# Optimization experiments

Measured on AMD Instinct MI355X. Metric: run time of the kernel, lower is better.

The kernel has to match this reference:

```python
import jax, jax.numpy as jnp
import numpy as np

K, D, BETA = 512, 64, 0.25


def conv(x, w, b, s, p):
    # x: NCHW, w: OIHW (torch Conv2d layout)
    y = jax.lax.conv_general_dilated(x, w, (s, s), [(p, p), (p, p)],
                                     dimension_numbers=('NCHW', 'OIHW', 'NCHW'))
    if b is not None:
        y = y + b[None, :, None, None]
    return y


def conv_t(x, w, b, s, p):
    # torch ConvTranspose2d: w is (Cin, Cout, k, k). Equivalent to a dilated conv
    # with flipped, transposed kernel and padding k-1-p.
    k = w.shape[2]
    w2 = jnp.transpose(jnp.flip(w, (2, 3)), (1, 0, 2, 3))  # -> (Cout, Cin, k, k)
    y = jax.lax.conv_general_dilated(x, w2, (1, 1), [(k - 1 - p, k - 1 - p)] * 2,
                                     lhs_dilation=(s, s),
                                     dimension_numbers=('NCHW', 'OIHW', 'NCHW'))
    return y + b[None, :, None, None]


def res_stack(x, w1s, w2s):
    # w1s: (n_blocks, C_mid, C_in, 3, 3); w2s: (n_blocks, C_in, C_mid, 1, 1); no bias
    for i in range(w1s.shape[0]):
        h = conv(jax.nn.relu(x), w1s[i], None, 1, 1)
        h = conv(jax.nn.relu(h), w2s[i], None, 1, 0)
        x = x + h
    return jax.nn.relu(x)


def setup_inputs() -> dict:
    key = jax.random.key(0)
    ks = jax.random.split(key, 24)
    rn = lambda k, shape, s=0.05: (jax.random.normal(k, shape, jnp.float32) * s)
    return {
        'x': jax.random.normal(ks[0], (64, 3, 128, 128), jnp.float32),
        'enc_w1': rn(ks[1], (64, 3, 4, 4)),    'enc_b1': rn(ks[2], (64,)),
        'enc_w2': rn(ks[3], (128, 64, 4, 4)),  'enc_b2': rn(ks[4], (128,)),
        'enc_w3': rn(ks[5], (128, 128, 3, 3)), 'enc_b3': rn(ks[6], (128,)),
        'enc_w4': rn(ks[7], (128, 128, 3, 3)), 'enc_b4': rn(ks[8], (128,)),
        'enc_res_w1': rn(ks[9], (2, 64, 128, 3, 3)),
        'enc_res_w2': rn(ks[10], (2, 128, 64, 1, 1)),
        'enc_adj_w': rn(ks[11], (64, 128, 1, 1)), 'enc_adj_b': rn(ks[12], (64,)),
        'E': jax.random.uniform(ks[13], (K, D), jnp.float32, -1.0 / K, 1.0 / K),
        'dec_adj_w': rn(ks[14], (128, 64, 3, 3)), 'dec_adj_b': rn(ks[15], (128,)),
        'dec_res_w1': rn(ks[16], (2, 64, 128, 3, 3)),
        'dec_res_w2': rn(ks[17], (2, 128, 64, 1, 1)),
        'tc1_w': rn(ks[18], (128, 64, 4, 4)), 'tc1_b': rn(ks[19], (64,)),
        'tc2_w': rn(ks[20], (64, 3, 4, 4)),  'tc2_b': rn(ks[21], (3,)),
    }


def vq_vae_forward(x, enc_w1, enc_b1, enc_w2, enc_b2, enc_w3, enc_b3, enc_w4, enc_b4,
                   enc_res_w1, enc_res_w2, enc_adj_w, enc_adj_b, E,
                   dec_adj_w, dec_adj_b, dec_res_w1, dec_res_w2, tc1_w, tc1_b, tc2_w, tc2_b):
    relu = jax.nn.relu
    # ---- Encoder ----
    h = relu(conv(x, enc_w1, enc_b1, 2, 1))      # (B,64,64,64)
    h = relu(conv(h, enc_w2, enc_b2, 2, 1))      # (B,128,32,32)
    h = relu(conv(h, enc_w3, enc_b3, 1, 1))
    h = conv(h, enc_w4, enc_b4, 1, 1)
    h = res_stack(h, enc_res_w1, enc_res_w2)
    Ze = conv(h, enc_adj_w, enc_adj_b, 1, 0)     # (B,D,32,32)
    # ---- Vector quantizer (eval mode, use_EMA=False) ----
    Zt = jnp.transpose(Ze, (0, 2, 3, 1))          # (B,H,W,D)
    flat = Zt.reshape(-1, D)                      # (N,D), N=65536
    dist = (jnp.sum(flat ** 2, axis=1, keepdims=True)
            + jnp.sum(E ** 2, axis=1)
            - 2.0 * flat @ E.T)                    # (N,K)
    idx = jnp.argmin(dist, axis=1)                # (N,)
    Zq = E[idx].reshape(Zt.shape)
    e_latent_loss = jnp.mean((jax.lax.stop_gradient(Zq) - Zt) ** 2)
    q_latent_loss = jnp.mean((Zq - jax.lax.stop_gradient(Zt)) ** 2)
    e_and_q = q_latent_loss + BETA * e_latent_loss
    Zq_st = Zt + jax.lax.stop_gradient(Zq - Zt)   # straight-through
    Zq_nchw = jnp.transpose(Zq_st, (0, 3, 1, 2))
    counts = jnp.zeros((K,), jnp.float32).at[idx].add(1.0)
    probs = counts / jnp.sum(counts)
    entropy_bits = -jnp.sum(probs * jnp.log2(probs + 1e-10))  # zero-count terms vanish
    est_words = 2.0 ** entropy_bits
    # ---- Decoder ----
    g = conv(Zq_nchw, dec_adj_w, dec_adj_b, 1, 1)  # (B,128,32,32)
    g = res_stack(g, dec_res_w1, dec_res_w2)
    g = relu(conv_t(g, tc1_w, tc1_b, 2, 1))        # (B,64,64,64)
    x_recon = conv_t(g, tc2_w, tc2_b, 2, 1)        # (B,3,128,128)
    return e_and_q, x_recon, e_latent_loss, q_latent_loss, est_words


def reference(x, enc_w1, enc_b1, enc_w2, enc_b2, enc_w3, enc_b3, enc_w4, enc_b4,
              enc_res_w1, enc_res_w2, enc_adj_w, enc_adj_b, E,
              dec_adj_w, dec_adj_b, dec_res_w1, dec_res_w2, tc1_w, tc1_b, tc2_w, tc2_b):
    return vq_vae_forward(x, enc_w1, enc_b1, enc_w2, enc_b2, enc_w3, enc_b3, enc_w4, enc_b4,
                          enc_res_w1, enc_res_w2, enc_adj_w, enc_adj_b, E,
                          dec_adj_w, dec_adj_b, dec_res_w1, dec_res_w2, tc1_w, tc1_b, tc2_w, tc2_b)
```

## Files before the change

kernel.cpp:

```cpp
#include <hip/hip_runtime.h>
#include <math.h>


typedef unsigned short u16;
typedef __attribute__((ext_vector_type(8))) short bf16x8;
typedef __attribute__((ext_vector_type(4))) float f32x4;

__device__ __forceinline__ float bf2f(u16 h) {
    union { unsigned u; float f; } v; v.u = ((unsigned)h) << 16; return v.f;
}
__device__ __forceinline__ u16 f2bf(float f) {
    union { float f; unsigned u; } v; v.f = f;
    unsigned r = v.u + 0x7FFFu + ((v.u >> 16) & 1u);
    return (u16)(r >> 16);
}
__device__ __forceinline__ unsigned relu2(unsigned x) {
    return x & ~(((x & 0x80008000u) >> 15) * 0xFFFFu);
}

template<int CIN, int COUT, int TAPMODE, bool RELU_IN, bool RELU_OUT,
         bool HAS_BIAS, bool RESID>
__global__ __launch_bounds__(256)
void mfma_conv_k(const u16* __restrict__ in, const u16* __restrict__ wT,
                 const float* __restrict__ bias, u16* __restrict__ out,
                 int Hin, int Win, int Hout, int Wout, int OS)
{
    constexpr int TM = 2, TN = 4;
    constexpr int LDA = 40;
    constexpr int NCH = CIN / 32;
    constexpr int NTAPS = (TAPMODE == 0) ? 1 : (TAPMODE == 1) ? 9
                        : (TAPMODE == 2) ? 16 : 4;
    constexpr int S = (TAPMODE == 2) ? 2 : 1;

    __shared__ alignas(16) u16 aT[128 * LDA];
    __shared__ alignas(16) u16 bT[64 * LDA];

    const int tid = threadIdx.x;
    const int m0 = blockIdx.x * 128;
    const int colbase = blockIdx.y << 6;
    const int pz = (TAPMODE == 3) ? blockIdx.z : 0;
    const u16* wTb = (TAPMODE == 3) ? wT + (size_t)pz * 4 * COUT * CIN : wT;
    const int oph = (TAPMODE == 3) ? (pz >> 1) : 0;
    const int opw = (TAPMODE == 3) ? (pz & 1) : 0;
    const int n_img = m0 >> 10;
    const int pixbase = m0 & 1023;

    const int r = tid >> 1, half = tid & 1;
    const int pr = pixbase + r;
    const int ohr = pr >> 5, owr = pr & 31;
    const u16* inb = in + (size_t)n_img * Hin * Win * CIN;

    const int wv = tid >> 6, lane = tid & 63;
    const int q = lane >> 4, l16 = lane & 15;
    const int mbase = wv * 32;
    const bool bload = r < 64;

    f32x4 acc[TM][TN] = {};

    const int total_it = NTAPS * NCH;
    uint4 pa0, pa1, pb0 = {0,0,0,0}, pb1 = {0,0,0,0};

#define LOAD_IT(IT) do {                                                        \
        int t_ = (IT) / NCH, cc_ = ((IT) % NCH) * 32;                           \
        int dh_, dw_;                                                           \
        if (TAPMODE == 0)      { dh_ = 0;              dw_ = 0; }               \
        else if (TAPMODE == 1) { dh_ = t_/3 - 1;       dw_ = t_%3 - 1; }        \
        else if (TAPMODE == 2) { dh_ = (t_>>2) - 1;    dw_ = (t_&3) - 1; }      \
        else                   { dh_ = (pz>>1) - (t_>>1); dw_ = (pz&1) - (t_&1); } \
        int ih_ = ohr * S + dh_;                                                \
        int iw_ = owr * S + dw_;                                                \
        bool ok_ = ((unsigned)ih_ < (unsigned)Hin) &&                           \
                   ((unsigned)iw_ < (unsigned)Win);                             \
        pa0 = (uint4){0,0,0,0}; pa1 = (uint4){0,0,0,0};                         \
        if (ok_) {                                                              \
            const u16* as_ = inb + ((size_t)ih_ * Win + iw_) * CIN              \
                             + half * 16 + cc_;                                 \
            pa0 = *(const uint4*)(as_);                                         \
            pa1 = *(const uint4*)(as_ + 8);                                     \
        }                                                                       \
        if (bload) {                                                            \
            const u16* bs_ = wTb + ((size_t)t_ * COUT + colbase + r) * CIN      \
                             + half * 16 + cc_;                                 \
            pb0 = *(const uint4*)(bs_);                                         \
            pb1 = *(const uint4*)(bs_ + 8);                                     \
        }                                                                       \
    } while (0)

    LOAD_IT(0);

    for (int it = 0; it < total_it; ++it) {
        __syncthreads();
        uint4 a0 = pa0, a1 = pa1;
        if (RELU_IN) {
            a0.x = relu2(a0.x); a0.y = relu2(a0.y); a0.z = relu2(a0.z); a0.w = relu2(a0.w);
            a1.x = relu2(a1.x); a1.y = relu2(a1.y); a1.z = relu2(a1.z); a1.w = relu2(a1.w);
        }
        *(uint4*)&aT[r * LDA + half * 16]     = a0;
        *(uint4*)&aT[r * LDA + half * 16 + 8] = a1;
        if (bload) {
            *(uint4*)&bT[r * LDA + half * 16]     = pb0;
            *(uint4*)&bT[r * LDA + half * 16 + 8] = pb1;
        }
        __syncthreads();
        if (it + 1 < total_it) LOAD_IT(it + 1);

        bf16x8 afr[TM], bfr[TN];
        #pragma unroll
        for (int tm = 0; tm < TM; ++tm)
            afr[tm] = *(const bf16x8*)&aT[(mbase + tm*16 + l16) * LDA + q * 8];
        #pragma unroll
        for (int tn = 0; tn < TN; ++tn)
            bfr[tn] = *(const bf16x8*)&bT[(tn*16 + l16) * LDA + q * 8];
        #pragma unroll
        for (int tm = 0; tm < TM; ++tm)
            #pragma unroll
            for (int tn = 0; tn < TN; ++tn)
                acc[tm][tn] = __builtin_amdgcn_mfma_f32_16x16x32_bf16(
                    afr[tm], bfr[tn], acc[tm][tn], 0, 0, 0);
    }
#undef LOAD_IT

    #pragma unroll
    for (int tm = 0; tm < TM; ++tm) {
        #pragma unroll
        for (int tn = 0; tn < TN; ++tn) {
            const int col = colbase + tn*16 + l16;
            const float bv = HAS_BIAS ? bias[col] : 0.0f;
            #pragma unroll
            for (int rg = 0; rg < 4; ++rg) {
                const int m = mbase + tm*16 + q*4 + rg;
                const int pix = pixbase + m;
                const int oh = pix >> 5, ow = pix & 31;
                size_t oidx = (((size_t)n_img * Hout + (oh*OS + oph)) * Wout
                               + (ow*OS + opw)) * COUT + col;
                float v = acc[tm][tn][rg] + bv;
                if (RESID) v += bf2f(out[oidx]);
                if (RELU_OUT) v = fmaxf(v, 0.0f);
                out[oidx] = f2bf(v);
            }
        }
    }
}

__global__ __launch_bounds__(256)
void res_fused_k(const u16* __restrict__ in, const u16* __restrict__ w1,
                 const u16* __restrict__ w2, u16* __restrict__ out)
{
    constexpr int LDA = 40;
    __shared__ alignas(16) u16 smem[20480];
    u16* aT   = smem;
    u16* bT   = smem + 5120;
    u16* mT0  = smem;
    u16* mT1  = smem + 5120;
    u16* b2T0 = smem + 10240;
    u16* b2T1 = smem + 15360;

    const int tid = threadIdx.x;
    const int m0 = blockIdx.x * 128;
    const int n_img = m0 >> 10;
    const int pixbase = m0 & 1023;

    const int r = tid >> 1, half = tid & 1;
    const int pr = pixbase + r;
    const int ohr = pr >> 5, owr = pr & 31;
    const u16* inb = in + (size_t)n_img * 1024 * 128;

    const int wv = tid >> 6, lane = tid & 63;
    const int q = lane >> 4, l16 = lane & 15;
    const int mbase = wv * 32;
    const bool bload = r < 64;

    {
        const u16* s = w2 + r * 64 + half * 32;
        u16* d = (half ? b2T1 : b2T0) + r * LDA;
        *(uint4*)(d)      = *(const uint4*)(s);
        *(uint4*)(d + 8)  = *(const uint4*)(s + 8);
        *(uint4*)(d + 16) = *(const uint4*)(s + 16);
        *(uint4*)(d + 24) = *(const uint4*)(s + 24);
    }

    f32x4 acc[2][4] = {};
    uint4 pa0, pa1, pb0 = {0,0,0,0}, pb1 = {0,0,0,0};

#define RLOAD(IT) do {                                                          \
        int t_ = (IT) >> 2, cc_ = ((IT) & 3) * 32;                              \
        int ih_ = ohr + t_/3 - 1, iw_ = owr + t_%3 - 1;                         \
        bool ok_ = ((unsigned)ih_ < 32u) && ((unsigned)iw_ < 32u);              \
        pa0 = (uint4){0,0,0,0}; pa1 = (uint4){0,0,0,0};                         \
        if (ok_) {                                                              \
            const u16* as_ = inb + ((size_t)ih_ * 32 + iw_) * 128               \
                             + half * 16 + cc_;                                 \
            pa0 = *(const uint4*)(as_);                                         \
            pa1 = *(const uint4*)(as_ + 8);                                     \
        }                                                                       \
        if (bload) {                                                            \
            const u16* bs_ = w1 + ((size_t)t_ * 64 + r) * 128                   \
                             + half * 16 + cc_;                                 \
            pb0 = *(const uint4*)(bs_);                                         \
            pb1 = *(const uint4*)(bs_ + 8);                                     \
        }                                                                       \
    } while (0)

    RLOAD(0);
    for (int it = 0; it < 36; ++it) {
        __syncthreads();
        uint4 a0 = pa0, a1 = pa1;
        a0.x = relu2(a0.x); a0.y = relu2(a0.y); a0.z = relu2(a0.z); a0.w = relu2(a0.w);
        a1.x = relu2(a1.x); a1.y = relu2(a1.y); a1.z = relu2(a1.z); a1.w = relu2(a1.w);
        *(uint4*)&aT[r * LDA + half * 16]     = a0;
        *(uint4*)&aT[r * LDA + half * 16 + 8] = a1;
        if (bload) {
            *(uint4*)&bT[r * LDA + half * 16]     = pb0;
            *(uint4*)&bT[r * LDA + half * 16 + 8] = pb1;
        }
        __syncthreads();
        if (it + 1 < 36) RLOAD(it + 1);

        bf16x8 afr[2], bfr[4];
        #pragma unroll
        for (int tm = 0; tm < 2; ++tm)
            afr[tm] = *(const bf16x8*)&aT[(mbase + tm*16 + l16) * LDA + q * 8];
        #pragma unroll
        for (int tn = 0; tn < 4; ++tn)
            bfr[tn] = *(const bf16x8*)&bT[(tn*16 + l16) * LDA + q * 8];
        #pragma unroll
        for (int tm = 0; tm < 2; ++tm)
            #pragma unroll
            for (int tn = 0; tn < 4; ++tn)
                acc[tm][tn] = __builtin_amdgcn_mfma_f32_16x16x32_bf16(
                    afr[tm], bfr[tn], acc[tm][tn], 0, 0, 0);
    }
#undef RLOAD

    __syncthreads();

    #pragma unroll
    for (int tm = 0; tm < 2; ++tm)
        #pragma unroll
        for (int tn = 0; tn < 4; ++tn) {
            u16* dst = (tn < 2) ? mT0 : mT1;
            const int kc = (tn & 1) * 16 + l16;
            #pragma unroll
            for (int rg = 0; rg < 4; ++rg) {
                int row = mbase + tm*16 + q*4 + rg;
                dst[row * LDA + kc] = f2bf(fmaxf(acc[tm][tn][rg], 0.0f));
            }
        }
    __syncthreads();

    f32x4 acc2[2][8] = {};
    #pragma unroll
    for (int kk = 0; kk < 2; ++kk) {
        const u16* mp = kk ? mT1 : mT0;
        const u16* bp = kk ? b2T1 : b2T0;
        bf16x8 af[2], bf[8];
        #pragma unroll
        for (int tm = 0; tm < 2; ++tm)
            af[tm] = *(const bf16x8*)&mp[(mbase + tm*16 + l16) * LDA + q * 8];
        #pragma unroll
        for (int tn = 0; tn < 8; ++tn)
            bf[tn] = *(const bf16x8*)&bp[(tn*16 + l16) * LDA + q * 8];
        #pragma unroll
        for (int tm = 0; tm < 2; ++tm)
            #pragma unroll
            for (int tn = 0; tn < 8; ++tn)
                acc2[tm][tn] = __builtin_amdgcn_mfma_f32_16x16x32_bf16(
                    af[tm], bf[tn], acc2[tm][tn], 0, 0, 0);
    }

    #pragma unroll
    for (int tm = 0; tm < 2; ++tm)
        #pragma unroll
        for (int tn = 0; tn < 8; ++tn) {
            const int col = tn*16 + l16;
            #pragma unroll
            for (int rg = 0; rg < 4; ++rg) {
                const int m = mbase + tm*16 + q*4 + rg;
                const int pix = pixbase + m;
                size_t off = ((size_t)n_img * 1024 + pix) * 128 + col;
                out[off] = f2bf(acc2[tm][tn][rg] + bf2f(in[off]));
            }
        }
}

__global__ __launch_bounds__(256)
void adjvq_k(const u16* __restrict__ TRin, const u16* __restrict__ wadj,
             const float* __restrict__ bias, const u16* __restrict__ Ebf,
             const float* __restrict__ enorm1, u16* __restrict__ Zq,
             u16* __restrict__ idx_out, float* __restrict__ sse)
{
    constexpr int LDA = 40;
    __shared__ alignas(16) u16 smem[18432];
    u16* aT  = smem;
    u16* bT  = smem + 5120;
    u16* mT0 = smem;
    u16* mT1 = smem + 5120;
    u16* eld = smem;
    __shared__ float znorm_s[128];
    __shared__ float bestf_s[128];
    __shared__ float en1s[256];
    __shared__ int   bestk_s[128];
    __shared__ float red[256];

    const int tid = threadIdx.x;
    const int r = tid >> 1, half = tid & 1;
    const size_t gp = (size_t)blockIdx.x * 128 + r;
    const u16* arow = TRin + gp * 128 + half * 16;
    const u16* brow = wadj + (size_t)r * 128 + half * 16;

    const int wv = tid >> 6, lane = tid & 63;
    const int q = lane >> 4, l16 = lane & 15;
    const int mbase = wv * 32;

    f32x4 acc[2][4] = {};
    for (int c0 = 0; c0 < 128; c0 += 32) {
        __syncthreads();
        uint4 a0 = *(const uint4*)(arow + c0);
        uint4 a1 = *(const uint4*)(arow + c0 + 8);
        a0.x = relu2(a0.x); a0.y = relu2(a0.y); a0.z = relu2(a0.z); a0.w = relu2(a0.w);
        a1.x = relu2(a1.x); a1.y = relu2(a1.y); a1.z = relu2(a1.z); a1.w = relu2(a1.w);
        *(uint4*)&aT[r * LDA + half * 16]     = a0;
        *(uint4*)&aT[r * LDA + half * 16 + 8] = a1;
        if (r < 64) {
            *(uint4*)&bT[r * LDA + half * 16]     = *(const uint4*)(brow + c0);
            *(uint4*)&bT[r * LDA + half * 16 + 8] = *(const uint4*)(brow + c0 + 8);
        }
        __syncthreads();
        bf16x8 afr[2], bfr[4];
        #pragma unroll
        for (int tm = 0; tm < 2; ++tm)
            afr[tm] = *(const bf16x8*)&aT[(mbase + tm*16 + l16) * LDA + q * 8];
        #pragma unroll
        for (int tn = 0; tn < 4; ++tn)
            bfr[tn] = *(const bf16x8*)&bT[(tn*16 + l16) * LDA + q * 8];
        #pragma unroll
        for (int tm = 0; tm < 2; ++tm)
            #pragma unroll
            for (int tn = 0; tn < 4; ++tn)
                acc[tm][tn] = __builtin_amdgcn_mfma_f32_16x16x32_bf16(
                    afr[tm], bfr[tn], acc[tm][tn], 0, 0, 0);
    }

    float zn[2][4] = {};
    #pragma unroll
    for (int tm = 0; tm < 2; ++tm)
        #pragma unroll
        for (int tn = 0; tn < 4; ++tn) {
            const float bv = bias[tn*16 + l16];
            #pragma unroll
            for (int rg = 0; rg < 4; ++rg) {
                float z = acc[tm][tn][rg] + bv;
                acc[tm][tn][rg] = z;
                zn[tm][rg] = fmaf(z, z, zn[tm][rg]);
            }
        }
    #pragma unroll
    for (int m = 1; m < 16; m <<= 1)
        #pragma unroll
        for (int tm = 0; tm < 2; ++tm)
            #pragma unroll
            for (int rg = 0; rg < 4; ++rg)
                zn[tm][rg] += __shfl_xor(zn[tm][rg], m, 64);

    __syncthreads();

    #pragma unroll
    for (int tm = 0; tm < 2; ++tm) {
        #pragma unroll
        for (int tn = 0; tn < 4; ++tn) {
            u16* dst = (tn < 2) ? mT0 : mT1;
            const int kc = (tn & 1) * 16 + l16;
            #pragma unroll
            for (int rg = 0; rg < 4; ++rg) {
                int row = mbase + tm*16 + q*4 + rg;
                dst[row * LDA + kc] = f2bf(acc[tm][tn][rg]);
            }
        }
        if (l16 == 0)
            #pragma unroll
            for (int rg = 0; rg < 4; ++rg)
                znorm_s[mbase + tm*16 + q*4 + rg] = zn[tm][rg];
    }
    __syncthreads();

    bf16x8 alo[2], ahi[2];
    #pragma unroll
    for (int tile = 0; tile < 2; ++tile) {
        alo[tile] = *(const bf16x8*)&mT0[(mbase + tile*16 + l16) * LDA + q * 8];
        ahi[tile] = *(const bf16x8*)&mT1[(mbase + tile*16 + l16) * LDA + q * 8];
    }

    unsigned key[2][4] = {{0xFFFFFFFFu,0xFFFFFFFFu,0xFFFFFFFFu,0xFFFFFFFFu},
                          {0xFFFFFFFFu,0xFFFFFFFFu,0xFFFFFFFFu,0xFFFFFFFFu}};
    float fb[2][4] = {{1e30f,1e30f,1e30f,1e30f},{1e30f,1e30f,1e30f,1e30f}};

    for (int k0 = 0; k0 < 512; k0 += 256) {
        __syncthreads();
        const uint4* src = (const uint4*)(Ebf + k0 * 64);
        #pragma unroll
        for (int i = tid; i < 2048; i += 256) {
            int row = i >> 3, sub = i & 7;
            *(uint4*)&eld[row * 72 + sub * 8] = src[i];
        }
        en1s[tid] = enorm1[k0 + tid];
        __syncthreads();

        for (int t = 0; t < 16; ++t) {
            const int nl = t * 16 + l16;
            bf16x8 b0 = *(const bf16x8*)&eld[nl * 72 + q * 8];
            bf16x8 b1 = *(const bf16x8*)&eld[nl * 72 + 32 + q * 8];
            const float en1 = en1s[nl];
            const unsigned ng = (unsigned)(k0 + nl);
            #pragma unroll
            for (int tile = 0; tile < 2; ++tile) {
                f32x4 sc4 = {0.0f, 0.0f, 0.0f, 0.0f};
                sc4 = __builtin_amdgcn_mfma_f32_16x16x32_bf16(alo[tile], b0, sc4, 0, 0, 0);
                sc4 = __builtin_amdgcn_mfma_f32_16x16x32_bf16(ahi[tile], b1, sc4, 0, 0, 0);
                #pragma unroll
                for (int rg = 0; rg < 4; ++rg) {
                    float sc = fmaf(sc4[rg], -2.0f, en1);
                    unsigned kk2 = (__float_as_uint(sc) & 0xFFFFFE00u) | ng;
                    key[tile][rg] = min(key[tile][rg], kk2);
                    fb[tile][rg] = fminf(fb[tile][rg], sc);
                }
            }
        }
    }

    #pragma unroll
    for (int m = 1; m < 16; m <<= 1)
        #pragma unroll
        for (int tile = 0; tile < 2; ++tile)
            #pragma unroll
            for (int rg = 0; rg < 4; ++rg) {
                unsigned o = (unsigned)__shfl_xor((int)key[tile][rg], m, 64);
                key[tile][rg] = min(key[tile][rg], o);
                float of = __shfl_xor(fb[tile][rg], m, 64);
                fb[tile][rg] = fminf(fb[tile][rg], of);
            }
    if (l16 == 0)
        #pragma unroll
        for (int tile = 0; tile < 2; ++tile)
            #pragma unroll
            for (int rg = 0; rg < 4; ++rg) {
                int row = mbase + tile*16 + q*4 + rg;
                bestk_s[row] = (int)(key[tile][rg] & 511u);
                bestf_s[row] = fb[tile][rg];
            }
    __syncthreads();

    const int pos = tid >> 1, seg = tid & 1;
    const size_t p = (size_t)blockIdx.x * 128 + pos;
    const int k = bestk_s[pos];
    const u16* ep = Ebf + (size_t)k * 64 + seg * 32;
    u16* qp = Zq + p * 64 + seg * 32;
    #pragma unroll
    for (int h = 0; h < 4; ++h)
        *(uint4*)(qp + h * 8) = *(const uint4*)(ep + h * 8);
    if (seg == 0) idx_out[p] = (u16)k;
    red[tid] = (seg == 0) ? (znorm_s[pos] + bestf_s[pos] - 1.0f) : 0.0f;
    __syncthreads();
    for (int s = 128; s > 0; s >>= 1) {
        if (tid < s) red[tid] += red[tid + s];
        __syncthreads();
    }
    if (tid == 0) atomicAdd(sse, red[0]);
}

__global__ __launch_bounds__(256)
void conv1_mfma_k(const float* __restrict__ x, const u16* __restrict__ wc1b,
                  const float* __restrict__ b, u16* __restrict__ out)
{
    __shared__ alignas(16) u16 smem[15360];
    u16* aT0 = smem;
    u16* aT1 = smem + 5120;
    u16* bT0 = smem + 10240;
    u16* bT1 = smem + 12800;

    const int tid = threadIdx.x;
    const int gbase = blockIdx.x * 128;
    const int r = tid >> 1, half = tid & 1;
    const int p = gbase + r;
    const int ow = p & 63, oh = (p >> 6) & 63, n = p >> 12;
    const float* xb = x + (size_t)n * 3 * 16384;

    {
        int row = tid >> 2, sub = tid & 3;
        *(uint4*)&bT0[row*40 + sub*8] = *(const uint4*)(wc1b + row*64 + sub*8);
        *(uint4*)&bT1[row*40 + sub*8] = *(const uint4*)(wc1b + row*64 + 32 + sub*8);
    }

    float vals[24];
    const int kb = half * 24;
    #pragma unroll
    for (int j = 0; j < 24; ++j) {
        int k = kb + j;
        int ci = k >> 4, kh = (k >> 2) & 3, kw = k & 3;
        int ih = oh*2 - 1 + kh, iw = ow*2 - 1 + kw;
        bool ok = ((unsigned)ih < 128u) && ((unsigned)iw < 128u);
        vals[j] = ok ? xb[ci*16384 + ih*128 + iw] : 0.0f;
    }
    unsigned pk[12];
    #pragma unroll
    for (int jj = 0; jj < 12; ++jj)
        pk[jj] = (unsigned)f2bf(vals[2*jj]) | ((unsigned)f2bf(vals[2*jj+1]) << 16);
    unsigned* a0row = (unsigned*)&aT0[r * 40];
    unsigned* a1row = (unsigned*)&aT1[r * 40];
    if (half == 0) {
        #pragma unroll
        for (int jj = 0; jj < 12; ++jj) a0row[jj] = pk[jj];
    } else {
        a0row[12] = pk[0]; a0row[13] = pk[1];
        a0row[14] = pk[2]; a0row[15] = pk[3];
        #pragma unroll
        for (int jj = 4; jj < 12; ++jj) a1row[jj - 4] = pk[jj];
        *(uint4*)&aT1[r*40 + 16] = (uint4){0,0,0,0};
        *(uint4*)&aT1[r*40 + 24] = (uint4){0,0,0,0};
    }
    __syncthreads();

    const int wv = tid >> 6, lane = tid & 63;
    const int q = lane >> 4, l16 = lane & 15;
    const int mbase = wv * 32;

    f32x4 acc[2][4] = {};
    bf16x8 af0[2], af1[2], bf0[4], bf1[4];
    #pragma unroll
    for (int tm = 0; tm < 2; ++tm) {
        af0[tm] = *(const bf16x8*)&aT0[(mbase + tm*16 + l16) * 40 + q * 8];
        af1[tm] = *(const bf16x8*)&aT1[(mbase + tm*16 + l16) * 40 + q * 8];
    }
    #pragma unroll
    for (int tn = 0; tn < 4; ++tn) {
        bf0[tn] = *(const bf16x8*)&bT0[(tn*16 + l16) * 40 + q * 8];
        bf1[tn] = *(const bf16x8*)&bT1[(tn*16 + l16) * 40 + q * 8];
    }
    #pragma unroll
    for (int tm = 0; tm < 2; ++tm)
        #pragma unroll
        for (int tn = 0; tn < 4; ++tn) {
            acc[tm][tn] = __builtin_amdgcn_mfma_f32_16x16x32_bf16(
                af0[tm], bf0[tn], acc[tm][tn], 0, 0, 0);
            acc[tm][tn] = __builtin_amdgcn_mfma_f32_16x16x32_bf16(
                af1[tm], bf1[tn], acc[tm][tn], 0, 0, 0);
        }

    float bv[4];
    #pragma unroll
    for (int tn = 0; tn < 4; ++tn) bv[tn] = b[tn*16 + l16];

    __syncthreads();
    u16* cbuf = smem;
    #pragma unroll
    for (int tm = 0; tm < 2; ++tm)
        #pragma unroll
        for (int tn = 0; tn < 4; ++tn)
            #pragma unroll
            for (int rg = 0; rg < 4; ++rg) {
                int row = mbase + tm*16 + q*4 + rg;
                int col = tn*16 + l16;
                cbuf[row*72 + col] = f2bf(fmaxf(acc[tm][tn][rg] + bv[tn], 0.0f));
            }
    __syncthreads();

    u16* ob = out + (size_t)gbase * 64;
    #pragma unroll
    for (int it = 0; it < 4; ++it) {
        int j = it * 256 + tid;
        uint4 v = *(const uint4*)&cbuf[(j >> 3) * 72 + (j & 7) * 8];
        *(uint4*)(ob + j * 8) = v;
    }
}

__global__ __launch_bounds__(256)
void tc2_mfma_k(const u16* __restrict__ in, const u16* __restrict__ wT,
                const float* __restrict__ bias, float* __restrict__ out)
{
    constexpr int LDA = 40;
    __shared__ alignas(16) u16 aT[128 * LDA];
    __shared__ alignas(16) u16 bT[16 * LDA];
    __shared__ float cT[128 * 17];

    const int tid = threadIdx.x;
    const int m0 = blockIdx.x * 128;
    const int n_img = m0 >> 12;
    const int pixbase = m0 & 4095;
    const int y0 = pixbase >> 6;

    const int r = tid >> 1, half = tid & 1;
    const int pr = pixbase + r;
    const int yr = pr >> 6, xr = pr & 63;
    const u16* inb = in + (size_t)n_img * 4096 * 64;

    const int wv = tid >> 6, lane = tid & 63;
    const int q = lane >> 4, l16 = lane & 15;
    const int mbase = wv * 32;

    f32x4 acc[2] = {};

    for (int t = 0; t < 9; ++t) {
        const int ih = yr + t/3 - 1;
        const int iw = xr + t%3 - 1;
        const bool ok = ((unsigned)ih < 64u) && ((unsigned)iw < 64u);
        const u16* asrc = ok ? (inb + ((size_t)ih * 64 + iw) * 64 + half * 16) : inb;
        const u16* bsrc = wT + ((size_t)t * 16 + r) * 64 + half * 16;

        for (int c0 = 0; c0 < 64; c0 += 32) {
            __syncthreads();
            uint4 a0 = {0,0,0,0}, a1 = {0,0,0,0};
            if (ok) {
                a0 = *(const uint4*)(asrc + c0);
                a1 = *(const uint4*)(asrc + c0 + 8);
            }
            *(uint4*)&aT[r * LDA + half * 16]     = a0;
            *(uint4*)&aT[r * LDA + half * 16 + 8] = a1;
            if (r < 16) {
                *(uint4*)&bT[r * LDA + half * 16]     = *(const uint4*)(bsrc + c0);
                *(uint4*)&bT[r * LDA + half * 16 + 8] = *(const uint4*)(bsrc + c0 + 8);
            }
            __syncthreads();

            bf16x8 af0 = *(const bf16x8*)&aT[(mbase + l16) * LDA + q * 8];
            bf16x8 af1 = *(const bf16x8*)&aT[(mbase + 16 + l16) * LDA + q * 8];
            bf16x8 bf  = *(const bf16x8*)&bT[l16 * LDA + q * 8];
            acc[0] = __builtin_amdgcn_mfma_f32_16x16x32_bf16(af0, bf, acc[0], 0, 0, 0);
            acc[1] = __builtin_amdgcn_mfma_f32_16x16x32_bf16(af1, bf, acc[1], 0, 0, 0);
        }
    }

    #pragma unroll
    for (int tm = 0; tm < 2; ++tm)
        #pragma unroll
        for (int rg = 0; rg < 4; ++rg)
            cT[(mbase + tm*16 + q*4 + rg) * 17 + l16] = acc[tm][rg];
    __syncthreads();

    #pragma unroll
    for (int it = 0; it < 6; ++it) {
        int j = it * 256 + tid;
        int co  = j >> 9;
        int rem = j & 511;
        int ohl = rem >> 7;
        int ow  = rem & 127;
        int oh  = 2*y0 + ohl;
        int lp  = (ohl >> 1) * 64 + (ow >> 1);
        int col = ((ohl & 1) * 2 + (ow & 1)) * 4 + co;
        float v = cT[lp * 17 + col] + bias[co];
        out[(((size_t)n_img * 3 + co) * 128 + oh) * 128 + ow] = v;
    }
}

__global__ __launch_bounds__(256)
void hist_k(const u16* __restrict__ idx, float* __restrict__ counts)
{
    __shared__ int red[256];
    const int k = blockIdx.x;
    const int tid = threadIdx.x;
    int c = 0;
    const uint4* p4 = (const uint4*)idx;
    for (int i = tid; i < 8192; i += 256) {
        uint4 v = p4[i];
        unsigned ua[4] = {v.x, v.y, v.z, v.w};
        #pragma unroll
        for (int j = 0; j < 4; ++j) {
            c += ((ua[j] & 0xFFFFu) == (unsigned)k);
            c += ((ua[j] >> 16)     == (unsigned)k);
        }
    }
    red[tid] = c;
    __syncthreads();
    for (int s = 128; s > 0; s >>= 1) {
        if (tid < s) red[tid] += red[tid + s];
        __syncthreads();
    }
    if (tid == 0) counts[k] = (float)red[0];
}

__device__ __forceinline__ void wconv_tf(const float* __restrict__ w,
                                         u16* __restrict__ o,
                                         int COUT, int CIN, int KK, int i)
{
    int ci = i % CIN; int t = i / CIN; int co = t % COUT; t /= COUT;
    o[i] = f2bf(w[(co*CIN + ci)*KK + t]);
}

__global__ __launch_bounds__(256)
void prep_k(const float* __restrict__ enc_w1, const float* __restrict__ enc_w2,
            const float* __restrict__ enc_w3, const float* __restrict__ enc_w4,
            const float* __restrict__ enc_res_w1, const float* __restrict__ enc_res_w2,
            const float* __restrict__ dec_res_w1, const float* __restrict__ dec_res_w2,
            const float* __restrict__ enc_adj_w, const float* __restrict__ dec_adj_w,
            const float* __restrict__ tc1_w, const float* __restrict__ tc2_w,
            const float* __restrict__ E,
            u16* __restrict__ wc1b, u16* __restrict__ wc2, u16* __restrict__ wc3,
            u16* __restrict__ wc4, u16* __restrict__ wer1, u16* __restrict__ wer2,
            u16* __restrict__ wdr1, u16* __restrict__ wdr2, u16* __restrict__ weadj,
            u16* __restrict__ wdadj, u16* __restrict__ wtc1, u16* __restrict__ wtc2b,
            u16* __restrict__ Ebf, float* __restrict__ enorm1, float* __restrict__ sse)
{
    const int b = blockIdx.x, tid = threadIdx.x;
    if (b < 512) {
        wconv_tf(enc_w2, wc2, 128, 64, 16, b * 256 + tid);
    } else if (b < 1088) {
        wconv_tf(enc_w3, wc3, 128, 128, 9, (b - 512) * 256 + tid);
    } else if (b < 1664) {
        wconv_tf(enc_w4, wc4, 128, 128, 9, (b - 1088) * 256 + tid);
    } else if (b < 2240) {
        int i = (b - 1664) * 256 + tid;
        int sub = i / 73728, rem = i - sub * 73728;
        wconv_tf(enc_res_w1 + sub * 73728, wer1 + sub * 73728, 64, 128, 9, rem);
    } else if (b < 2816) {
        int i = (b - 2240) * 256 + tid;
        int sub = i / 73728, rem = i - sub * 73728;
        wconv_tf(dec_res_w1 + sub * 73728, wdr1 + sub * 73728, 64, 128, 9, rem);
    } else if (b < 2880) {
        int i = (b - 2816) * 256 + tid;
        int sub = i >> 13, rem = i & 8191;
        wconv_tf(enc_res_w2 + sub * 8192, wer2 + sub * 8192, 128, 64, 1, rem);
    } else if (b < 2944) {
        int i = (b - 2880) * 256 + tid;
        int sub = i >> 13, rem = i & 8191;
        wconv_tf(dec_res_w2 + sub * 8192, wdr2 + sub * 8192, 128, 64, 1, rem);
    } else if (b < 2976) {
        wconv_tf(enc_adj_w, weadj, 64, 128, 1, (b - 2944) * 256 + tid);
    } else if (b < 3264) {
        wconv_tf(dec_adj_w, wdadj, 128, 64, 9, (b - 2976) * 256 + tid);
    } else if (b < 3776) {
        int i = (b - 3264) * 256 + tid;
        int ci = i & 127; int co = (i >> 7) & 63; int t = (i >> 13) & 3; int p = i >> 15;
        int poh = p >> 1, pw = p & 1; int a = t >> 1, bb = t & 1;
        int kh = poh ? (a ? 2 : 0) : (a ? 3 : 1);
        int kw = pw  ? (bb ? 2 : 0) : (bb ? 3 : 1);
        wtc1[i] = f2bf(tc1_w[((ci*64 + co)*4 + kh)*4 + kw]);
    } else if (b < 3812) {
        int i = (b - 3776) * 256 + tid;
        int ci = i & 63; int col = (i >> 6) & 15; int t = i >> 10;
        int dh = t / 3 - 1, dw = t % 3 - 1;
        int pp = col >> 2, co = col & 3;
        float v = 0.0f;
        if (co < 3) {
            int poh = pp >> 1, pw = pp & 1;
            int kh = poh ? (dh == 1 ? 0 : (dh == 0 ? 2 : -1))
                         : (dh == 0 ? 1 : (dh == -1 ? 3 : -1));
            int kw = pw  ? (dw == 1 ? 0 : (dw == 0 ? 2 : -1))
                         : (dw == 0 ? 1 : (dw == -1 ? 3 : -1));
            if (kh >= 0 && kw >= 0)
                v = tc2_w[((ci*3 + co)*4 + kh)*4 + kw];
        }
        wtc2b[i] = f2bf(v);
    } else if (b < 3814) {
        int k = (b - 3812) * 256 + tid;
        float s = 0.0f;
        #pragma unroll
        for (int d = 0; d < 64; ++d) {
            u16 h = f2bf(E[k*64 + d]);
            Ebf[k*64 + d] = h;
            float v = bf2f(h);
            s = fmaf(v, v, s);
        }
        enorm1[k] = s + 1.0f;
    } else if (b < 3830) {
        int i = (b - 3814) * 256 + tid;
        int co = i >> 6, k = i & 63;
        float v = 0.0f;
        if (k < 48) {
            int ci = k >> 4, kh = (k >> 2) & 3, kw = k & 3;
            v = enc_w1[((co*3 + ci)*4 + kh)*4 + kw];
        }
        wc1b[i] = f2bf(v);
    } else {
        if (tid == 0) sse[0] = 0.0f;
    }
}

__global__ void finalize_k(const float* __restrict__ counts, const float* __restrict__ sse,
                           float* __restrict__ out_head, float* __restrict__ out_tail)
{
    __shared__ float red[512];
    int t = threadIdx.x;
    float pr = counts[t] / 65536.0f;
    red[t] = -pr * log2f(pr + 1e-10f);
    __syncthreads();
    for (int s = 256; s > 0; s >>= 1) {
        if (t < s) red[t] += red[t + s];
        __syncthreads();
    }
    if (t == 0) {
        float entropy = red[0];
        float mse = sse[0] / 4194304.0f;
        out_head[0] = 1.25f * mse;
        out_tail[0] = mse;
        out_tail[1] = mse;
        out_tail[2] = exp2f(entropy);
    }
}

extern "C" void kernel_launch(void* const* d_in, const int* in_sizes, int n_in,
                              void* d_out, int out_size, void* d_ws, size_t ws_size,
                              hipStream_t stream)
{
    const float* x         = (const float*)d_in[0];
    const float* enc_w1    = (const float*)d_in[1];
    const float* enc_b1    = (const float*)d_in[2];
    const float* enc_w2    = (const float*)d_in[3];
    const float* enc_b2    = (const float*)d_in[4];
    const float* enc_w3    = (const float*)d_in[5];
    const float* enc_b3    = (const float*)d_in[6];
    const float* enc_w4    = (const float*)d_in[7];
    const float* enc_b4    = (const float*)d_in[8];
    const float* enc_res_w1= (const float*)d_in[9];
    const float* enc_res_w2= (const float*)d_in[10];
    const float* enc_adj_w = (const float*)d_in[11];
    const float* enc_adj_b = (const float*)d_in[12];
    const float* Ecb       = (const float*)d_in[13];
    const float* dec_adj_w = (const float*)d_in[14];
    const float* dec_adj_b = (const float*)d_in[15];
    const float* dec_res_w1= (const float*)d_in[16];
    const float* dec_res_w2= (const float*)d_in[17];
    const float* tc1_w     = (const float*)d_in[18];
    const float* tc1_b     = (const float*)d_in[19];
    const float* tc2_w     = (const float*)d_in[20];
    const float* tc2_b     = (const float*)d_in[21];

    char* wsb = (char*)d_ws;
    u16*   wc2   = (u16*)(wsb + 0);
    u16*   wc3   = (u16*)(wsb + 262144);
    u16*   wc4   = (u16*)(wsb + 557056);
    u16*   wer1  = (u16*)(wsb + 851968);
    u16*   wer2  = (u16*)(wsb + 1146880);
    u16*   weadj = (u16*)(wsb + 1179648);
    u16*   wdadj = (u16*)(wsb + 1196032);
    u16*   wdr1  = (u16*)(wsb + 1343488);
    u16*   wdr2  = (u16*)(wsb + 1638400);
    u16*   wtc1  = (u16*)(wsb + 1671168);
    u16*   wtc2b = (u16*)(wsb + 1933312);
    float* counts= (float*)(wsb + 1951744);
    float* sse   = counts + 512;
    u16*   Ebf   = (u16*)(wsb + 1955840);
    float* enorm1= (float*)(wsb + 2021376);
    u16*   wc1b  = (u16*)(wsb + 2023424);
    u16*   H1    = (u16*)(wsb + 2097152);
    u16*   TR    = (u16*)(wsb + 35651584);
    u16*   H3    = (u16*)(wsb + 52428800);
    u16*   ZQ    = (u16*)(wsb + 85983232);
    u16*   IDX   = (u16*)(wsb + 94371840);
    u16*   TC1O  = H1;

    float* out  = (float*)d_out;
    float* xrec = out + 1;
    float* tail = out + 1 + 3145728;

    prep_k<<<3831, 256, 0, stream>>>(enc_w1, enc_w2, enc_w3, enc_w4,
        enc_res_w1, enc_res_w2, dec_res_w1, dec_res_w2, enc_adj_w, dec_adj_w,
        tc1_w, tc2_w, Ecb, wc1b, wc2, wc3, wc4, wer1, wer2, wdr1, wdr2,
        weadj, wdadj, wtc1, wtc2b, Ebf, enorm1, sse);

    conv1_mfma_k<<<2048, 256, 0, stream>>>(x, wc1b, enc_b1, H1);
    mfma_conv_k<64,128,2,false,true,true,false><<<dim3(512,2), 256, 0, stream>>>
        (H1, wc2, enc_b2, TR, 64, 64, 32, 32, 1);
    mfma_conv_k<128,128,1,false,true,true,false><<<dim3(512,2), 256, 0, stream>>>
        (TR, wc3, enc_b3, H3, 32, 32, 32, 32, 1);
    mfma_conv_k<128,128,1,false,false,true,false><<<dim3(512,2), 256, 0, stream>>>
        (H3, wc4, enc_b4, TR, 32, 32, 32, 32, 1);
    res_fused_k<<<512, 256, 0, stream>>>(TR, wer1,         wer2,        H3);
    res_fused_k<<<512, 256, 0, stream>>>(H3, wer1 + 73728, wer2 + 8192, TR);

    adjvq_k<<<512, 256, 0, stream>>>(TR, weadj, enc_adj_b, Ebf, enorm1,
                                     ZQ, IDX, sse);
    hist_k<<<512, 256, 0, stream>>>(IDX, counts);

    mfma_conv_k<64,128,1,false,false,true,false><<<dim3(512,2), 256, 0, stream>>>
        (ZQ, wdadj, dec_adj_b, H3, 32, 32, 32, 32, 1);
    res_fused_k<<<512, 256, 0, stream>>>(H3, wdr1,         wdr2,        TR);
    res_fused_k<<<512, 256, 0, stream>>>(TR, wdr1 + 73728, wdr2 + 8192, H3);
    mfma_conv_k<128,64,3,true,true,true,false><<<dim3(512,1,4), 256, 0, stream>>>
        (H3, wtc1, tc1_b, TC1O, 32, 32, 64, 64, 2);
    tc2_mfma_k<<<2048, 256, 0, stream>>>(TC1O, wtc2b, tc2_b, xrec);

    finalize_k<<<1, 512, 0, stream>>>(counts, sse, out, tail);
}
```

Measured before the change: 450.6 us.

## Double-buffer LDS tiles in conv MFMA kernels to drop one barrier per step

Three MFMA conv kernels (generic conv, fused residual and tc2) now keep two LDS staging buffers. The next tile is written to the alternate buffer while the current one feeds the MFMAs, and the global load runs two iterations ahead, so each iteration needs one barrier instead of two. tc2 also gets register prefetch, which it lacked before. LDS use grows, and this may lower occupancy for the residual kernel. Register pressure also rises from holding prefetched data longer.

```diff
diff --git a/kernel.cpp b/kernel.cpp
--- a/kernel.cpp
+++ b/kernel.cpp
@@ -32,8 +32,8 @@
                         : (TAPMODE == 2) ? 16 : 4;
     constexpr int S = (TAPMODE == 2) ? 2 : 1;
 
-    __shared__ alignas(16) u16 aT[128 * LDA];
-    __shared__ alignas(16) u16 bT[64 * LDA];
+    __shared__ alignas(16) u16 aT[2][128 * LDA];
+    __shared__ alignas(16) u16 bT[2][64 * LDA];
 
     const int tid = threadIdx.x;
     const int m0 = blockIdx.x * 128;
@@ -86,38 +86,47 @@
         }                                                                       \
     } while (0)
 
+#define STORE_STAGE(BUF) do {                                                   \
+        uint4 a0 = pa0, a1 = pa1;                                               \
+        if (RELU_IN) {                                                          \
+            a0.x = relu2(a0.x); a0.y = relu2(a0.y);                             \
+            a0.z = relu2(a0.z); a0.w = relu2(a0.w);                             \
+            a1.x = relu2(a1.x); a1.y = relu2(a1.y);                             \
+            a1.z = relu2(a1.z); a1.w = relu2(a1.w);                             \
+        }                                                                       \
+        *(uint4*)&aT[BUF][r * LDA + half * 16]     = a0;                        \
+        *(uint4*)&aT[BUF][r * LDA + half * 16 + 8] = a1;                        \
+        if (bload) {                                                            \
+            *(uint4*)&bT[BUF][r * LDA + half * 16]     = pb0;                   \
+            *(uint4*)&bT[BUF][r * LDA + half * 16 + 8] = pb1;                   \
+        }                                                                       \
+    } while (0)
+
     LOAD_IT(0);
+    STORE_STAGE(0);
+    LOAD_IT(1);
+    __syncthreads();
 
     for (int it = 0; it < total_it; ++it) {
-        __syncthreads();
-        uint4 a0 = pa0, a1 = pa1;
-        if (RELU_IN) {
-            a0.x = relu2(a0.x); a0.y = relu2(a0.y); a0.z = relu2(a0.z); a0.w = relu2(a0.w);
-            a1.x = relu2(a1.x); a1.y = relu2(a1.y); a1.z = relu2(a1.z); a1.w = relu2(a1.w);
-        }
-        *(uint4*)&aT[r * LDA + half * 16]     = a0;
-        *(uint4*)&aT[r * LDA + half * 16 + 8] = a1;
-        if (bload) {
-            *(uint4*)&bT[r * LDA + half * 16]     = pb0;
-            *(uint4*)&bT[r * LDA + half * 16 + 8] = pb1;
-        }
-        __syncthreads();
-        if (it + 1 < total_it) LOAD_IT(it + 1);
-
+        const int cur = it & 1;
         bf16x8 afr[TM], bfr[TN];
         #pragma unroll
         for (int tm = 0; tm < TM; ++tm)
-            afr[tm] = *(const bf16x8*)&aT[(mbase + tm*16 + l16) * LDA + q * 8];
+            afr[tm] = *(const bf16x8*)&aT[cur][(mbase + tm*16 + l16) * LDA + q * 8];
         #pragma unroll
         for (int tn = 0; tn < TN; ++tn)
-            bfr[tn] = *(const bf16x8*)&bT[(tn*16 + l16) * LDA + q * 8];
+            bfr[tn] = *(const bf16x8*)&bT[cur][(tn*16 + l16) * LDA + q * 8];
+        if (it + 1 < total_it) STORE_STAGE(cur ^ 1);
+        if (it + 2 < total_it) LOAD_IT(it + 2);
         #pragma unroll
         for (int tm = 0; tm < TM; ++tm)
             #pragma unroll
             for (int tn = 0; tn < TN; ++tn)
                 acc[tm][tn] = __builtin_amdgcn_mfma_f32_16x16x32_bf16(
                     afr[tm], bfr[tn], acc[tm][tn], 0, 0, 0);
-    }
+        if (it + 1 < total_it) __syncthreads();
+    }
+#undef STORE_STAGE
 #undef LOAD_IT
 
     #pragma unroll
@@ -147,13 +156,15 @@
                  const u16* __restrict__ w2, u16* __restrict__ out)
 {
     constexpr int LDA = 40;
-    __shared__ alignas(16) u16 smem[20480];
-    u16* aT   = smem;
-    u16* bT   = smem + 5120;
+    __shared__ alignas(16) u16 smem[25600];
+    u16* aT0  = smem;
+    u16* aT1  = smem + 5120;
+    u16* bT0  = smem + 10240;
+    u16* bT1  = smem + 12800;
+    u16* b2T0 = smem + 15360;
+    u16* b2T1 = smem + 20480;
     u16* mT0  = smem;
     u16* mT1  = smem + 5120;
-    u16* b2T0 = smem + 10240;
-    u16* b2T1 = smem + 15360;
 
     const int tid = threadIdx.x;
     const int m0 = blockIdx.x * 128;
@@ -201,35 +212,49 @@
         }                                                                       \
     } while (0)
 
+#define RSTORE(BUF) do {                                                        \
+        u16* aD_ = (BUF) ? aT1 : aT0;                                           \
+        u16* bD_ = (BUF) ? bT1 : bT0;                                           \
+        uint4 a0 = pa0, a1 = pa1;                                               \
+        a0.x = relu2(a0.x); a0.y = relu2(a0.y);                                 \
+        a0.z = relu2(a0.z); a0.w = relu2(a0.w);                                 \
+        a1.x = relu2(a1.x); a1.y = relu2(a1.y);                                 \
+        a1.z = relu2(a1.z); a1.w = relu2(a1.w);                                 \
+        *(uint4*)&aD_[r * LDA + half * 16]     = a0;                            \
+        *(uint4*)&aD_[r * LDA + half * 16 + 8] = a1;                            \
+        if (bload) {                                                            \
+            *(uint4*)&bD_[r * LDA + half * 16]     = pb0;                       \
+            *(uint4*)&bD_[r * LDA + half * 16 + 8] = pb1;                       \
+        }                                                                       \
+    } while (0)
+
     RLOAD(0);
+    RSTORE(0);
+    RLOAD(1);
+    __syncthreads();
+
     for (int it = 0; it < 36; ++it) {
-        __syncthreads();
-        uint4 a0 = pa0, a1 = pa1;
-        a0.x = relu2(a0.x); a0.y = relu2(a0.y); a0.z = relu2(a0.z); a0.w = relu2(a0.w);
-        a1.x = relu2(a1.x); a1.y = relu2(a1.y); a1.z = relu2(a1.z); a1.w = relu2(a1.w);
-        *(uint4*)&aT[r * LDA + half * 16]     = a0;
-        *(uint4*)&aT[r * LDA + half * 16 + 8] = a1;
-        if (bload) {
-            *(uint4*)&bT[r * LDA + half * 16]     = pb0;
-            *(uint4*)&bT[r * LDA + half * 16 + 8] = pb1;
-        }
-        __syncthreads();
-        if (it + 1 < 36) RLOAD(it + 1);
-
+        const int cur = it & 1;
+        const u16* aC = cur ? aT1 : aT0;
+        const u16* bC = cur ? bT1 : bT0;
         bf16x8 afr[2], bfr[4];
         #pragma unroll
         for (int tm = 0; tm < 2; ++tm)
-            afr[tm] = *(const bf16x8*)&aT[(mbase + tm*16 + l16) * LDA + q * 8];
+            afr[tm] = *(const bf16x8*)&aC[(mbase + tm*16 + l16) * LDA + q * 8];
         #pragma unroll
         for (int tn = 0; tn < 4; ++tn)
-            bfr[tn] = *(const bf16x8*)&bT[(tn*16 + l16) * LDA + q * 8];
+            bfr[tn] = *(const bf16x8*)&bC[(tn*16 + l16) * LDA + q * 8];
+        if (it + 1 < 36) RSTORE(cur ^ 1);
+        if (it + 2 < 36) RLOAD(it + 2);
         #pragma unroll
         for (int tm = 0; tm < 2; ++tm)
             #pragma unroll
             for (int tn = 0; tn < 4; ++tn)
                 acc[tm][tn] = __builtin_amdgcn_mfma_f32_16x16x32_bf16(
                     afr[tm], bfr[tn], acc[tm][tn], 0, 0, 0);
-    }
+        if (it + 1 < 36) __syncthreads();
+    }
+#undef RSTORE
 #undef RLOAD
 
     __syncthreads();
@@ -577,9 +602,12 @@
                 const float* __restrict__ bias, float* __restrict__ out)
 {
     constexpr int LDA = 40;
-    __shared__ alignas(16) u16 aT[128 * LDA];
-    __shared__ alignas(16) u16 bT[16 * LDA];
-    __shared__ float cT[128 * 17];
+    __shared__ alignas(16) u16 smem[11520];
+    u16* aT0 = smem;
+    u16* aT1 = smem + 5120;
+    u16* bT0 = smem + 10240;
+    u16* bT1 = smem + 10880;
+    float* cT = (float*)smem;
 
     const int tid = threadIdx.x;
     const int m0 = blockIdx.x * 128;
@@ -597,36 +625,59 @@
     const int mbase = wv * 32;
 
     f32x4 acc[2] = {};
-
-    for (int t = 0; t < 9; ++t) {
-        const int ih = yr + t/3 - 1;
-        const int iw = xr + t%3 - 1;
-        const bool ok = ((unsigned)ih < 64u) && ((unsigned)iw < 64u);
-        const u16* asrc = ok ? (inb + ((size_t)ih * 64 + iw) * 64 + half * 16) : inb;
-        const u16* bsrc = wT + ((size_t)t * 16 + r) * 64 + half * 16;
-
-        for (int c0 = 0; c0 < 64; c0 += 32) {
-            __syncthreads();
-            uint4 a0 = {0,0,0,0}, a1 = {0,0,0,0};
-            if (ok) {
-                a0 = *(const uint4*)(asrc + c0);
-                a1 = *(const uint4*)(asrc + c0 + 8);
-            }
-            *(uint4*)&aT[r * LDA + half * 16]     = a0;
-            *(uint4*)&aT[r * LDA + half * 16 + 8] = a1;
-            if (r < 16) {
-                *(uint4*)&bT[r * LDA + half * 16]     = *(const uint4*)(bsrc + c0);
-                *(uint4*)&bT[r * LDA + half * 16 + 8] = *(const uint4*)(bsrc + c0 + 8);
-            }
-            __syncthreads();
-
-            bf16x8 af0 = *(const bf16x8*)&aT[(mbase + l16) * LDA + q * 8];
-            bf16x8 af1 = *(const bf16x8*)&aT[(mbase + 16 + l16) * LDA + q * 8];
-            bf16x8 bf  = *(const bf16x8*)&bT[l16 * LDA + q * 8];
-            acc[0] = __builtin_amdgcn_mfma_f32_16x16x32_bf16(af0, bf, acc[0], 0, 0, 0);
-            acc[1] = __builtin_amdgcn_mfma_f32_16x16x32_bf16(af1, bf, acc[1], 0, 0, 0);
-        }
-    }
+    uint4 pa0, pa1, pb0 = {0,0,0,0}, pb1 = {0,0,0,0};
+
+#define TLOAD(IT) do {                                                          \
+        int t_ = (IT) >> 1, c0_ = ((IT) & 1) * 32;                              \
+        int ih_ = yr + t_/3 - 1, iw_ = xr + t_%3 - 1;                           \
+        bool ok_ = ((unsigned)ih_ < 64u) && ((unsigned)iw_ < 64u);              \
+        pa0 = (uint4){0,0,0,0}; pa1 = (uint4){0,0,0,0};                         \
+        if (ok_) {                                                              \
+            const u16* as_ = inb + ((size_t)ih_ * 64 + iw_) * 64                \
+                             + half * 16 + c0_;                                 \
+            pa0 = *(const uint4*)(as_);                                         \
+            pa1 = *(const uint4*)(as_ + 8);                                     \
+        }                                                                       \
+        if (r < 16) {                                                           \
+            const u16* bs_ = wT + ((size_t)t_ * 16 + r) * 64 + half * 16 + c0_; \
+            pb0 = *(const uint4*)(bs_);                                         \
+            pb1 = *(const uint4*)(bs_ + 8);                                     \
+        }                                                                       \
+    } while (0)
+
+#define TSTORE(BUF) do {                                                        \
+        u16* aD_ = (BUF) ? aT1 : aT0;                                           \
+        u16* bD_ = (BUF) ? bT1 : bT0;                                           \
+        *(uint4*)&aD_[r * LDA + half * 16]     = pa0;                           \
+        *(uint4*)&aD_[r * LDA + half * 16 + 8] = pa1;                           \
+        if (r < 16) {                                                           \
+            *(uint4*)&bD_[r * LDA + half * 16]     = pb0;                       \
+            *(uint4*)&bD_[r * LDA + half * 16 + 8] = pb1;                       \
+        }                                                                       \
+    } while (0)
+
+    TLOAD(0);
+    TSTORE(0);
+    TLOAD(1);
+    __syncthreads();
+
+    for (int it = 0; it < 18; ++it) {
+        const int cur = it & 1;
+        const u16* aC = cur ? aT1 : aT0;
+        const u16* bC = cur ? bT1 : bT0;
+        bf16x8 af0 = *(const bf16x8*)&aC[(mbase + l16) * LDA + q * 8];
+        bf16x8 af1 = *(const bf16x8*)&aC[(mbase + 16 + l16) * LDA + q * 8];
+        bf16x8 bf  = *(const bf16x8*)&bC[l16 * LDA + q * 8];
+        if (it + 1 < 18) TSTORE(cur ^ 1);
+        if (it + 2 < 18) TLOAD(it + 2);
+        acc[0] = __builtin_amdgcn_mfma_f32_16x16x32_bf16(af0, bf, acc[0], 0, 0, 0);
+        acc[1] = __builtin_amdgcn_mfma_f32_16x16x32_bf16(af1, bf, acc[1], 0, 0, 0);
+        if (it + 1 < 18) __syncthreads();
+    }
+#undef TSTORE
+#undef TLOAD
+
+    __syncthreads();
 
     #pragma unroll
     for (int tm = 0; tm < 2; ++tm)
```

After: 457.4 us. No clear change (+1.5%).
